# Kernel optimization log

Measured on AMD Instinct MI355X. Metric: run time of the kernel, lower is better.

## Reference

```python
import jax, jax.numpy as jnp
import numpy as np

B, H, N, D = 4, 16, 1024, 64


def setup_inputs() -> dict:
    key = jax.random.key(0)
    k1, k2, k3, k4, k5 = jax.random.split(key, 5)
    q = jax.random.normal(k1, (B, H, N, D), dtype=jnp.float32)
    k = jax.random.normal(k2, (B, H, N, D), dtype=jnp.float32)
    v = jax.random.normal(k3, (B, H, N, D), dtype=jnp.float32)
    # 1x1 Conv2d(heads, heads) weights -> [out_heads, in_heads]
    fan = 1.0 / np.sqrt(H)
    W_pre = jax.random.uniform(k4, (H, H), dtype=jnp.float32, minval=-fan, maxval=fan)
    W_post = jax.random.uniform(k5, (H, H), dtype=jnp.float32, minval=-fan, maxval=fan)
    return {"q": q, "k": k, "v": v, "W_pre": W_pre, "W_post": W_post}


def reference(q, k, v, W_pre, W_post):
    # q,k,v: [b, h, n, d]; talking-heads 1x1 conv mixes the head dim.
    scale = q.shape[-1] ** -0.5
    dots = jnp.einsum('bhid,bhjd->bhij', q, k) * scale
    # pre-softmax talking heads: out[g] = sum_h W_pre[g,h] * dots[h]
    dots = jnp.einsum('gh,bhij->bgij', W_pre, dots)
    n = dots.shape[-1]
    mask_value = -jnp.finfo(dots.dtype).max
    causal_mask = jnp.triu(jnp.ones((n, n), dtype=bool), k=1)  # [i, j]
    dots = jnp.where(causal_mask, mask_value, dots)
    # softmax computed in fp32 (qk_norm=False path), cast back to input dtype
    attn = jax.nn.softmax(dots.astype(jnp.float32), axis=-1).astype(dots.dtype)
    # post-softmax talking heads
    attn = jnp.einsum('gh,bhij->bgij', W_post, attn)
    out = jnp.einsum('bhij,bhjd->bhid', attn, v)
    return out
```

## Files before the change

### kernel.cpp

```cpp
#include <hip/hip_runtime.h>
#include <stdint.h>

#define B_  4
#define H_  16
#define N_  1024
#define D_  64
#define SS_R 328
#define A2_R 328

typedef _Float16 half4v __attribute__((ext_vector_type(4)));
typedef _Float16 half8v __attribute__((ext_vector_type(8)));
typedef float    f32x4  __attribute__((ext_vector_type(4)));

#define VT_OFF   0
#define VT_SZ    (B_ * H_ * D_ * N_ * 2)
#define LB_OFF   (VT_OFF + VT_SZ)
#define LB_SZ    (B_ * H_ * N_ * 4)
#define E_OFF    (LB_OFF + LB_SZ)
#define E_SZ     ((size_t)B_ * 2080 * 4096 * 2)
#define WS_NEED  ((size_t)E_OFF + E_SZ)

__device__ __forceinline__ half4v cvt4(f32x4 v) {
    half4v h;
    h[0] = (_Float16)v[0]; h[1] = (_Float16)v[1];
    h[2] = (_Float16)v[2]; h[3] = (_Float16)v[3];
    return h;
}

__device__ __forceinline__ int xcd_slot(int x) { return (x >> 3) + (x & 7) * 64; }

__global__ __launch_bounds__(256)
void prep_vt(const float* __restrict__ v, _Float16* __restrict__ VT) {
    __shared__ float T[64 * 67];
    const int t = threadIdx.x;
    const int bh = blockIdx.x >> 4, jb = blockIdx.x & 15, j0 = jb * 64;
    const float* src = v + ((size_t)bh * N_ + j0) * D_;
    #pragma unroll
    for (int m = 0; m < 4; ++m) {
        const int flat = m * 1024 + t * 4;
        const int j = flat >> 6, d0 = flat & 63;
        f32x4 val = *(const f32x4*)(src + flat);
        #pragma unroll
        for (int e = 0; e < 4; ++e) T[j * 67 + d0 + e] = val[e];
    }
    __syncthreads();
    const int d = t >> 2, jq = t & 3;
    half8v a, b2;
    #pragma unroll
    for (int jj = 0; jj < 8; ++jj) a[jj]  = (_Float16)T[(16 * jq + jj) * 67 + d];
    #pragma unroll
    for (int jj = 0; jj < 8; ++jj) b2[jj] = (_Float16)T[(16 * jq + 8 + jj) * 67 + d];
    _Float16* dst = VT + ((size_t)bh * D_ + d) * N_ + j0 + jq * 16;
    *(half8v*)dst = a;
    *(half8v*)(dst + 8) = b2;
}

__global__ __launch_bounds__(512, 2)
void attend_sweep1(const float* __restrict__ q, const float* __restrict__ k,
                   const float* __restrict__ Wpre, float* __restrict__ lbuf,
                   _Float16* __restrict__ Ebuf) {
    __shared__ _Float16 Ss[2][32 * SS_R];

    const int slot = xcd_slot(blockIdx.x);
    const int b = slot >> 7;
    const int r7 = slot & 127;
    const int m = r7 >> 2, phase = r7 & 3;
    const int itA = m, itB = 63 - m;
    const int i0A = m * 16, i0B = itB * 16;
    const int triA = itA * (itA + 1) / 2, triB = itB * (itB + 1) / 2;

    const int t = threadIdx.x;
    const int lane = t & 63, w = t >> 6;
    const int l16 = lane & 15, lg = lane >> 4;
    const int h0 = 2 * w;
    const size_t bh0 = (size_t)b * H_;
    _Float16* Eb = Ebuf + (size_t)b * 2080 * 4096;

    const half4v wpre_f = cvt4(*(const f32x4*)(Wpre + l16 * 16 + 4 * lg));

    half4v qf[2][2][4];
    #pragma unroll
    for (int s = 0; s < 2; ++s) {
        const int i0s = s ? i0B : i0A;
        #pragma unroll
        for (int e = 0; e < 2; ++e) {
            const float* qrow = q + ((bh0 + h0 + e) * N_ + i0s + l16) * D_;
            #pragma unroll
            for (int kk = 0; kk < 4; ++kk) {
                f32x4 qv = *(const f32x4*)(qrow + kk * 16 + 4 * lg);
                half4v hv;
                #pragma unroll
                for (int xx = 0; xx < 4; ++xx) hv[xx] = (_Float16)(qv[xx] * 0.125f);
                qf[s][e][kk] = hv;
            }
        }
    }

    float lp[4][4];
    #pragma unroll
    for (int ss = 0; ss < 4; ++ss)
        #pragma unroll
        for (int r = 0; r < 4; ++r) lp[ss][r] = 0.f;

    const float* kbase0 = k + ((bh0 + h0 + 0) * N_ + l16) * D_ + 4 * lg;
    const float* kbase1 = k + ((bh0 + h0 + 1) * N_ + l16) * D_ + 4 * lg;

    #define JT_OF(m_) (2 * (phase + 4 * ((m_) >> 1)) + ((m_) & 1))

    int jt = JT_OF(0);
    if (jt <= itB) {
        int pbuf = 0;
        half4v kfc[2][4];
        #pragma unroll
        for (int kk = 0; kk < 4; ++kk) {
            kfc[0][kk] = cvt4(*(const f32x4*)(kbase0 + (size_t)jt * 16 * D_ + kk * 16));
            kfc[1][kk] = cvt4(*(const f32x4*)(kbase1 + (size_t)jt * 16 * D_ + kk * 16));
        }
        for (int m_ = 0; ; ++m_) {
            const bool actA = (jt <= itA);
            #pragma unroll
            for (int s = 0; s < 2; ++s) {
                if (s == 0 && !actA) continue;
                #pragma unroll
                for (int e = 0; e < 2; ++e) {
                    f32x4 acc = {0.f, 0.f, 0.f, 0.f};
                    #pragma unroll
                    for (int kk = 0; kk < 4; ++kk)
                        acc = __builtin_amdgcn_mfma_f32_16x16x16f16(qf[s][e][kk], kfc[e][kk], acc, 0, 0, 0);
                    #pragma unroll
                    for (int r = 0; r < 4; ++r)
                        Ss[pbuf][(s * 16 + 4 * lg + r) * SS_R + l16 * 20 + h0 + e] = (_Float16)acc[r];
                }
            }
            const int jn = JT_OF(m_ + 1);
            const bool have_next = (jn <= itB);
            half4v kfn[2][4];
            if (have_next) {
                #pragma unroll
                for (int kk = 0; kk < 4; ++kk) {
                    kfn[0][kk] = cvt4(*(const f32x4*)(kbase0 + (size_t)jn * 16 * D_ + kk * 16));
                    kfn[1][kk] = cvt4(*(const f32x4*)(kbase1 + (size_t)jn * 16 * D_ + kk * 16));
                }
            }
            __syncthreads();
            #pragma unroll
            for (int ss = 0; ss < 4; ++ss) {
                const int strip = ss >> 1;
                if (strip == 0 && !actA) continue;
                const int sii = (ss & 1) * 8 + w;
                const int its = strip ? itB : itA;
                const int tri = strip ? triB : triA;
                half4v sfrag = *(const half4v*)&Ss[pbuf][(strip * 16 + sii) * SS_R + l16 * 20 + 4 * lg];
                f32x4 z = {0.f, 0.f, 0.f, 0.f};
                f32x4 m1 = __builtin_amdgcn_mfma_f32_16x16x16f16(wpre_f, sfrag, z, 0, 0, 0);
                const bool ok = (jt < its) || (l16 <= sii);
                half4v ev;
                #pragma unroll
                for (int r = 0; r < 4; ++r) {
                    const float e_ = ok ? __expf(m1[r]) : 0.f;
                    lp[ss][r] += e_;
                    ev[r] = (_Float16)e_;
                }
                *(half4v*)(Eb + (size_t)(tri + jt) * 4096 + w * 512 + l16 * 32 + lg * 8 + (ss & 1) * 4) = ev;
            }
            pbuf ^= 1;
            if (!have_next) break;
            jt = jn;
            #pragma unroll
            for (int kk = 0; kk < 4; ++kk) {
                kfc[0][kk] = kfn[0][kk];
                kfc[1][kk] = kfn[1][kk];
            }
        }
    }
    #undef JT_OF

    #pragma unroll
    for (int ss = 0; ss < 4; ++ss) {
        const int strip = ss >> 1;
        const int sii = (ss & 1) * 8 + w;
        const int i0s = strip ? i0B : i0A;
        #pragma unroll
        for (int r = 0; r < 4; ++r) {
            float val = lp[ss][r];
            val += __shfl_xor(val, 1, 64);
            val += __shfl_xor(val, 2, 64);
            val += __shfl_xor(val, 4, 64);
            val += __shfl_xor(val, 8, 64);
            if (l16 == 0)
                atomicAdd(&lbuf[(bh0 + 4 * lg + r) * N_ + i0s + sii], val);
        }
    }
}

__global__ __launch_bounds__(512, 8)
void attend_sweep2(const _Float16* __restrict__ Ebuf, const _Float16* __restrict__ VT,
                   const float* __restrict__ Wpost, const float* __restrict__ lbuf,
                   float* __restrict__ out) {
    __shared__ _Float16 A2s[2][16 * A2_R];

    const int x = blockIdx.x;
    const int r_ = x >> 4;
    const int it = (r_ < 32) ? (63 - r_) : (r_ - 32);
    const int sub = x & 15;
    const int b = sub >> 2, dq = sub & 3;
    const int i0 = it * 16;

    const int t = threadIdx.x;
    const int lane = t & 63, w = t >> 6;
    const int l16 = lane & 15, lg = lane >> 4;
    const int h0 = 2 * w;
    const size_t bh0 = (size_t)b * H_;

    const half4v wpost_f = cvt4(*(const f32x4*)(Wpost + l16 * 16 + 4 * lg));

    float lrecip[2][4];
    #pragma unroll
    for (int ss = 0; ss < 2; ++ss) {
        const int sii = ss * 8 + w;
        #pragma unroll
        for (int r = 0; r < 4; ++r)
            lrecip[ss][r] = 1.0f / lbuf[(bh0 + 4 * lg + r) * N_ + i0 + sii];
    }

    const _Float16* Eb = Ebuf + ((size_t)b * 2080 + (size_t)it * (it + 1) / 2) * 4096
                       + w * 512 + l16 * 32 + lg * 8;
    const _Float16* vb0 = VT + ((bh0 + h0 + 0) * D_ + dq * 16 + l16) * (size_t)N_ + 4 * lg;
    const _Float16* vb1 = VT + ((bh0 + h0 + 1) * D_ + dq * 16 + l16) * (size_t)N_ + 4 * lg;

    f32x4 oacc[2];
    #pragma unroll
    for (int e = 0; e < 2; ++e) oacc[e] = (f32x4){0.f, 0.f, 0.f, 0.f};

    int pb = 0;
    half8v e0 = *(const half8v*)(Eb);
    half8v e1 = (it >= 1) ? *(const half8v*)(Eb + 4096) : e0;
    half4v vc[2];
    vc[0] = *(const half4v*)(vb0);
    vc[1] = *(const half4v*)(vb1);

    for (int jt = 0; jt <= it; ++jt) {
        half8v e2 = e1;
        if (jt + 2 <= it) e2 = *(const half8v*)(Eb + (size_t)(jt + 2) * 4096);
        half4v vn[2];
        if (jt + 1 <= it) {
            vn[0] = *(const half4v*)(vb0 + (jt + 1) * 16);
            vn[1] = *(const half4v*)(vb1 + (jt + 1) * 16);
        } else {
            vn[0] = vc[0]; vn[1] = vc[1];
        }
        #pragma unroll
        for (int ss = 0; ss < 2; ++ss) {
            const int sii = ss * 8 + w;
            half4v pf;
            #pragma unroll
            for (int r = 0; r < 4; ++r)
                pf[r] = (_Float16)((float)e0[ss * 4 + r] * lrecip[ss][r]);
            f32x4 z = {0.f, 0.f, 0.f, 0.f};
            f32x4 m2 = __builtin_amdgcn_mfma_f32_16x16x16f16(wpost_f, pf, z, 0, 0, 0);
            #pragma unroll
            for (int r = 0; r < 4; ++r)
                A2s[pb][(4 * lg + r) * A2_R + sii * 20 + l16] = (_Float16)m2[r];
        }
        __syncthreads();
        #pragma unroll
        for (int e = 0; e < 2; ++e) {
            const int g = h0 + e;
            half4v bfrag = *(const half4v*)&A2s[pb][g * A2_R + l16 * 20 + 4 * lg];
            oacc[e] = __builtin_amdgcn_mfma_f32_16x16x16f16(vc[e], bfrag, oacc[e], 0, 0, 0);
        }
        e0 = e1; e1 = e2;
        vc[0] = vn[0]; vc[1] = vn[1];
        pb ^= 1;
    }

    #pragma unroll
    for (int e = 0; e < 2; ++e) {
        float* orow = out + ((bh0 + h0 + e) * N_ + i0 + l16) * D_;
        *(f32x4*)&orow[dq * 16 + 4 * lg] = oacc[e];
    }
}

__global__ __launch_bounds__(512, 2)
void attend_fused(const float* __restrict__ q, const float* __restrict__ k,
                  const float* __restrict__ v, const float* __restrict__ Wpre,
                  const float* __restrict__ Wpost, float* __restrict__ out) {
    __shared__ _Float16 Ss[32 * SS_R];
    __shared__ _Float16 A2s[16 * 648];

    const int t = threadIdx.x;
    const int b = blockIdx.x >> 5;
    const int m = blockIdx.x & 31;
    const int itA = m, itB = 63 - m;
    const int i0A = m * 16, i0B = (63 - m) * 16;

    const int lane = t & 63, w = t >> 6;
    const int l16 = lane & 15, lg = lane >> 4;
    const int h0 = 2 * w;
    const size_t bh0 = (size_t)b * H_;

    const half4v wpre_f  = cvt4(*(const f32x4*)(Wpre  + l16 * 16 + 4 * lg));
    const half4v wpost_f = cvt4(*(const f32x4*)(Wpost + l16 * 16 + 4 * lg));

    half4v qf[2][2][4];
    #pragma unroll
    for (int s = 0; s < 2; ++s) {
        const int i0s = s ? i0B : i0A;
        #pragma unroll
        for (int e = 0; e < 2; ++e) {
            const float* qrow = q + ((bh0 + h0 + e) * N_ + i0s + l16) * D_;
            #pragma unroll
            for (int kk = 0; kk < 4; ++kk) {
                f32x4 qv = *(const f32x4*)(qrow + kk * 16 + 4 * lg);
                half4v hv;
                #pragma unroll
                for (int xx = 0; xx < 4; ++xx) hv[xx] = (_Float16)(qv[xx] * 0.125f);
                qf[s][e][kk] = hv;
            }
        }
    }

    float lp[4][4];
    #pragma unroll
    for (int ss = 0; ss < 4; ++ss)
        #pragma unroll
        for (int r = 0; r < 4; ++r) lp[ss][r] = 0.f;

    for (int jt = 0; jt <= itB; ++jt) {
        const int j0 = jt * 16;
        const bool actA = (jt <= itA);
        half4v kf[2][4];
        #pragma unroll
        for (int e = 0; e < 2; ++e) {
            const float* krow = k + ((bh0 + h0 + e) * N_ + j0 + l16) * D_ + 4 * lg;
            #pragma unroll
            for (int kk = 0; kk < 4; ++kk) kf[e][kk] = cvt4(*(const f32x4*)(krow + kk * 16));
        }
        #pragma unroll
        for (int s = 0; s < 2; ++s) {
            if (s == 0 && !actA) continue;
            #pragma unroll
            for (int e = 0; e < 2; ++e) {
                f32x4 acc = {0.f, 0.f, 0.f, 0.f};
                #pragma unroll
                for (int kk = 0; kk < 4; ++kk)
                    acc = __builtin_amdgcn_mfma_f32_16x16x16f16(qf[s][e][kk], kf[e][kk], acc, 0, 0, 0);
                #pragma unroll
                for (int r = 0; r < 4; ++r)
                    Ss[(s * 16 + 4 * lg + r) * SS_R + l16 * 20 + h0 + e] = (_Float16)acc[r];
            }
        }
        __syncthreads();
        #pragma unroll
        for (int ss = 0; ss < 4; ++ss) {
            const int strip = ss >> 1;
            if (strip == 0 && !actA) continue;
            const int sii = (ss & 1) * 8 + w;
            const int its = strip ? itB : itA;
            half4v sfrag = *(const half4v*)&Ss[(strip * 16 + sii) * SS_R + l16 * 20 + 4 * lg];
            f32x4 z = {0.f, 0.f, 0.f, 0.f};
            f32x4 m1 = __builtin_amdgcn_mfma_f32_16x16x16f16(wpre_f, sfrag, z, 0, 0, 0);
            if ((jt < its) || (l16 <= sii)) {
                #pragma unroll
                for (int r = 0; r < 4; ++r) lp[ss][r] += __expf(m1[r]);
            }
        }
        __syncthreads();
    }

    float lrec[4][4];
    #pragma unroll
    for (int ss = 0; ss < 4; ++ss)
        #pragma unroll
        for (int r = 0; r < 4; ++r) {
            float val = lp[ss][r];
            val += __shfl_xor(val, 1, 64);
            val += __shfl_xor(val, 2, 64);
            val += __shfl_xor(val, 4, 64);
            val += __shfl_xor(val, 8, 64);
            lrec[ss][r] = 1.0f / val;
        }

    f32x4 oacc[2][2][4];
    #pragma unroll
    for (int s = 0; s < 2; ++s)
        #pragma unroll
        for (int e = 0; e < 2; ++e)
            #pragma unroll
            for (int ds = 0; ds < 4; ++ds)
                oacc[s][e][ds] = (f32x4){0.f, 0.f, 0.f, 0.f};

    for (int jt = 0; jt <= itB; ++jt) {
        const int j0 = jt * 16;
        const bool actA = (jt <= itA);
        half4v kf[2][4];
        #pragma unroll
        for (int e = 0; e < 2; ++e) {
            const float* krow = k + ((bh0 + h0 + e) * N_ + j0 + l16) * D_ + 4 * lg;
            #pragma unroll
            for (int kk = 0; kk < 4; ++kk) kf[e][kk] = cvt4(*(const f32x4*)(krow + kk * 16));
        }
        half4v vf[2][4];
        #pragma unroll
        for (int e = 0; e < 2; ++e)
            #pragma unroll
            for (int ds = 0; ds < 4; ++ds) {
                f32x4 vv;
                #pragma unroll
                for (int xx = 0; xx < 4; ++xx)
                    vv[xx] = v[((bh0 + h0 + e) * N_ + j0 + 4 * lg + xx) * D_ + ds * 16 + l16];
                vf[e][ds] = cvt4(vv);
            }
        #pragma unroll
        for (int s = 0; s < 2; ++s) {
            if (s == 0 && !actA) continue;
            #pragma unroll
            for (int e = 0; e < 2; ++e) {
                f32x4 acc = {0.f, 0.f, 0.f, 0.f};
                #pragma unroll
                for (int kk = 0; kk < 4; ++kk)
                    acc = __builtin_amdgcn_mfma_f32_16x16x16f16(qf[s][e][kk], kf[e][kk], acc, 0, 0, 0);
                #pragma unroll
                for (int r = 0; r < 4; ++r)
                    Ss[(s * 16 + 4 * lg + r) * SS_R + l16 * 20 + h0 + e] = (_Float16)acc[r];
            }
        }
        __syncthreads();
        #pragma unroll
        for (int ss = 0; ss < 4; ++ss) {
            const int strip = ss >> 1;
            if (strip == 0 && !actA) continue;
            const int sii = (ss & 1) * 8 + w;
            const int its = strip ? itB : itA;
            half4v sfrag = *(const half4v*)&Ss[(strip * 16 + sii) * SS_R + l16 * 20 + 4 * lg];
            f32x4 z = {0.f, 0.f, 0.f, 0.f};
            f32x4 m1 = __builtin_amdgcn_mfma_f32_16x16x16f16(wpre_f, sfrag, z, 0, 0, 0);
            const bool ok = (jt < its) || (l16 <= sii);
            half4v pfrag;
            #pragma unroll
            for (int r = 0; r < 4; ++r)
                pfrag[r] = (_Float16)(ok ? __expf(m1[r]) * lrec[ss][r] : 0.f);
            f32x4 m2 = __builtin_amdgcn_mfma_f32_16x16x16f16(wpost_f, pfrag, z, 0, 0, 0);
            #pragma unroll
            for (int r = 0; r < 4; ++r)
                A2s[(4 * lg + r) * 648 + (strip * 16 + sii) * 20 + l16] = (_Float16)m2[r];
        }
        __syncthreads();
        #pragma unroll
        for (int s = 0; s < 2; ++s) {
            if (s == 0 && !actA) continue;
            #pragma unroll
            for (int e = 0; e < 2; ++e) {
                half4v bfrag = *(const half4v*)&A2s[(h0 + e) * 648 + (s * 16 + l16) * 20 + 4 * lg];
                #pragma unroll
                for (int ds = 0; ds < 4; ++ds)
                    oacc[s][e][ds] = __builtin_amdgcn_mfma_f32_16x16x16f16(vf[e][ds], bfrag, oacc[s][e][ds], 0, 0, 0);
            }
        }
    }

    #pragma unroll
    for (int s = 0; s < 2; ++s) {
        const int i0s = s ? i0B : i0A;
        #pragma unroll
        for (int e = 0; e < 2; ++e) {
            float* orow = out + ((bh0 + h0 + e) * N_ + i0s + l16) * D_;
            #pragma unroll
            for (int ds = 0; ds < 4; ++ds)
                *(f32x4*)&orow[ds * 16 + 4 * lg] = oacc[s][e][ds];
        }
    }
}

extern "C" void kernel_launch(void* const* d_in, const int* in_sizes, int n_in,
                              void* d_out, int out_size, void* d_ws, size_t ws_size,
                              hipStream_t stream) {
    const float* q     = (const float*)d_in[0];
    const float* k     = (const float*)d_in[1];
    const float* v     = (const float*)d_in[2];
    const float* Wpre  = (const float*)d_in[3];
    const float* Wpost = (const float*)d_in[4];
    float* out = (float*)d_out;
    _Float16* VT   = (_Float16*)((char*)d_ws + VT_OFF);
    float*    lbuf = (float*)((char*)d_ws + LB_OFF);
    _Float16* Ebuf = (_Float16*)((char*)d_ws + E_OFF);

    if (ws_size >= WS_NEED) {
        prep_vt<<<dim3(B_ * H_ * (N_ / 64)), dim3(256), 0, stream>>>(v, VT);
        hipMemsetAsync((char*)d_ws + LB_OFF, 0, LB_SZ, stream);
        attend_sweep1<<<dim3(512), dim3(512), 0, stream>>>(q, k, Wpre, lbuf, Ebuf);
        attend_sweep2<<<dim3(1024), dim3(512), 0, stream>>>(Ebuf, VT, Wpost, lbuf, out);
    } else {
        attend_fused<<<dim3(B_ * 32), dim3(512), 0, stream>>>(q, k, v, Wpre, Wpost, out);
    }
}
```

Measured before the change: 164.0 us.

## Pair causal row tiles in sweep2 to share V loads and balance work

Each sweep2 block now handles two query row tiles, m and 63-m, so every block does the same amount of causal work. The two tiles reuse the same V fragment loads and share one barrier per iteration, and the grid is halved to 512 blocks. The change removes the load imbalance between short and long rows and cuts redundant V traffic. In exchange it doubles LDS usage and register pressure, lowers the occupancy hint to 4, and drops the two-deep E prefetch and the V prefetch in favour of single-step lookahead.

```diff
diff --git a/kernel.cpp b/kernel.cpp
--- a/kernel.cpp
+++ b/kernel.cpp
@@ -193,18 +193,20 @@
     }
 }
 
-__global__ __launch_bounds__(512, 8)
+__global__ __launch_bounds__(512, 4)
 void attend_sweep2(const _Float16* __restrict__ Ebuf, const _Float16* __restrict__ VT,
                    const float* __restrict__ Wpost, const float* __restrict__ lbuf,
                    float* __restrict__ out) {
-    __shared__ _Float16 A2s[2][16 * A2_R];
+    __shared__ _Float16 A2sA[2][16 * A2_R];
+    __shared__ _Float16 A2sB[2][16 * A2_R];
 
     const int x = blockIdx.x;
-    const int r_ = x >> 4;
-    const int it = (r_ < 32) ? (63 - r_) : (r_ - 32);
+    const int xm = x >> 4;
+    const int m = (x < 256) ? xm : (31 - (xm & 15));
     const int sub = x & 15;
     const int b = sub >> 2, dq = sub & 3;
-    const int i0 = it * 16;
+    const int itA = m, itB = 63 - m;
+    const int i0A = m * 16, i0B = itB * 16;
 
     const int t = threadIdx.x;
     const int lane = t & 63, w = t >> 6;
@@ -214,70 +216,95 @@
 
     const half4v wpost_f = cvt4(*(const f32x4*)(Wpost + l16 * 16 + 4 * lg));
 
-    float lrecip[2][4];
+    float lrA[2][4], lrB[2][4];
     #pragma unroll
     for (int ss = 0; ss < 2; ++ss) {
         const int sii = ss * 8 + w;
         #pragma unroll
-        for (int r = 0; r < 4; ++r)
-            lrecip[ss][r] = 1.0f / lbuf[(bh0 + 4 * lg + r) * N_ + i0 + sii];
-    }
-
-    const _Float16* Eb = Ebuf + ((size_t)b * 2080 + (size_t)it * (it + 1) / 2) * 4096
-                       + w * 512 + l16 * 32 + lg * 8;
+        for (int r = 0; r < 4; ++r) {
+            lrA[ss][r] = 1.0f / lbuf[(bh0 + 4 * lg + r) * N_ + i0A + sii];
+            lrB[ss][r] = 1.0f / lbuf[(bh0 + 4 * lg + r) * N_ + i0B + sii];
+        }
+    }
+
+    const size_t lane_off = (size_t)w * 512 + l16 * 32 + lg * 8;
+    const _Float16* EbA = Ebuf + ((size_t)b * 2080 + (size_t)itA * (itA + 1) / 2) * 4096 + lane_off;
+    const _Float16* EbB = Ebuf + ((size_t)b * 2080 + (size_t)itB * (itB + 1) / 2) * 4096 + lane_off;
     const _Float16* vb0 = VT + ((bh0 + h0 + 0) * D_ + dq * 16 + l16) * (size_t)N_ + 4 * lg;
     const _Float16* vb1 = VT + ((bh0 + h0 + 1) * D_ + dq * 16 + l16) * (size_t)N_ + 4 * lg;
 
-    f32x4 oacc[2];
-    #pragma unroll
-    for (int e = 0; e < 2; ++e) oacc[e] = (f32x4){0.f, 0.f, 0.f, 0.f};
+    f32x4 oaccA[2], oaccB[2];
+    #pragma unroll
+    for (int e = 0; e < 2; ++e) {
+        oaccA[e] = (f32x4){0.f, 0.f, 0.f, 0.f};
+        oaccB[e] = (f32x4){0.f, 0.f, 0.f, 0.f};
+    }
 
     int pb = 0;
-    half8v e0 = *(const half8v*)(Eb);
-    half8v e1 = (it >= 1) ? *(const half8v*)(Eb + 4096) : e0;
-    half4v vc[2];
-    vc[0] = *(const half4v*)(vb0);
-    vc[1] = *(const half4v*)(vb1);
-
-    for (int jt = 0; jt <= it; ++jt) {
-        half8v e2 = e1;
-        if (jt + 2 <= it) e2 = *(const half8v*)(Eb + (size_t)(jt + 2) * 4096);
-        half4v vn[2];
-        if (jt + 1 <= it) {
-            vn[0] = *(const half4v*)(vb0 + (jt + 1) * 16);
-            vn[1] = *(const half4v*)(vb1 + (jt + 1) * 16);
-        } else {
-            vn[0] = vc[0]; vn[1] = vc[1];
-        }
+    half8v eB = *(const half8v*)(EbB);
+    half8v eA = *(const half8v*)(EbA);
+
+    for (int jt = 0; jt <= itB; ++jt) {
+        const bool actA = (jt <= itA);
+        half4v vf[2];
+        vf[0] = *(const half4v*)(vb0 + jt * 16);
+        vf[1] = *(const half4v*)(vb1 + jt * 16);
+        half8v eBn = eB, eAn = eA;
+        if (jt < itB) eBn = *(const half8v*)(EbB + (size_t)(jt + 1) * 4096);
+        if (jt < itA) eAn = *(const half8v*)(EbA + (size_t)(jt + 1) * 4096);
         #pragma unroll
         for (int ss = 0; ss < 2; ++ss) {
             const int sii = ss * 8 + w;
             half4v pf;
             #pragma unroll
             for (int r = 0; r < 4; ++r)
-                pf[r] = (_Float16)((float)e0[ss * 4 + r] * lrecip[ss][r]);
+                pf[r] = (_Float16)((float)eB[ss * 4 + r] * lrB[ss][r]);
             f32x4 z = {0.f, 0.f, 0.f, 0.f};
             f32x4 m2 = __builtin_amdgcn_mfma_f32_16x16x16f16(wpost_f, pf, z, 0, 0, 0);
             #pragma unroll
             for (int r = 0; r < 4; ++r)
-                A2s[pb][(4 * lg + r) * A2_R + sii * 20 + l16] = (_Float16)m2[r];
+                A2sB[pb][(4 * lg + r) * A2_R + sii * 20 + l16] = (_Float16)m2[r];
+        }
+        if (actA) {
+            #pragma unroll
+            for (int ss = 0; ss < 2; ++ss) {
+                const int sii = ss * 8 + w;
+                half4v pf;
+                #pragma unroll
+                for (int r = 0; r < 4; ++r)
+                    pf[r] = (_Float16)((float)eA[ss * 4 + r] * lrA[ss][r]);
+                f32x4 z = {0.f, 0.f, 0.f, 0.f};
+                f32x4 m2 = __builtin_amdgcn_mfma_f32_16x16x16f16(wpost_f, pf, z, 0, 0, 0);
+                #pragma unroll
+                for (int r = 0; r < 4; ++r)
+                    A2sA[pb][(4 * lg + r) * A2_R + sii * 20 + l16] = (_Float16)m2[r];
+            }
         }
         __syncthreads();
         #pragma unroll
         for (int e = 0; e < 2; ++e) {
             const int g = h0 + e;
-            half4v bfrag = *(const half4v*)&A2s[pb][g * A2_R + l16 * 20 + 4 * lg];
-            oacc[e] = __builtin_amdgcn_mfma_f32_16x16x16f16(vc[e], bfrag, oacc[e], 0, 0, 0);
-        }
-        e0 = e1; e1 = e2;
-        vc[0] = vn[0]; vc[1] = vn[1];
+            half4v bfB = *(const half4v*)&A2sB[pb][g * A2_R + l16 * 20 + 4 * lg];
+            oaccB[e] = __builtin_amdgcn_mfma_f32_16x16x16f16(vf[e], bfB, oaccB[e], 0, 0, 0);
+        }
+        if (actA) {
+            #pragma unroll
+            for (int e = 0; e < 2; ++e) {
+                const int g = h0 + e;
+                half4v bfA = *(const half4v*)&A2sA[pb][g * A2_R + l16 * 20 + 4 * lg];
+                oaccA[e] = __builtin_amdgcn_mfma_f32_16x16x16f16(vf[e], bfA, oaccA[e], 0, 0, 0);
+            }
+        }
+        eB = eBn; eA = eAn;
         pb ^= 1;
     }
 
     #pragma unroll
     for (int e = 0; e < 2; ++e) {
-        float* orow = out + ((bh0 + h0 + e) * N_ + i0 + l16) * D_;
-        *(f32x4*)&orow[dq * 16 + 4 * lg] = oacc[e];
+        float* orowB = out + ((bh0 + h0 + e) * N_ + i0B + l16) * D_;
+        *(f32x4*)&orowB[dq * 16 + 4 * lg] = oaccB[e];
+        float* orowA = out + ((bh0 + h0 + e) * N_ + i0A + l16) * D_;
+        *(f32x4*)&orowA[dq * 16 + 4 * lg] = oaccA[e];
     }
 }
 
@@ -489,7 +516,7 @@
         prep_vt<<<dim3(B_ * H_ * (N_ / 64)), dim3(256), 0, stream>>>(v, VT);
         hipMemsetAsync((char*)d_ws + LB_OFF, 0, LB_SZ, stream);
         attend_sweep1<<<dim3(512), dim3(512), 0, stream>>>(q, k, Wpre, lbuf, Ebuf);
-        attend_sweep2<<<dim3(1024), dim3(512), 0, stream>>>(Ebuf, VT, Wpost, lbuf, out);
+        attend_sweep2<<<dim3(512), dim3(512), 0, stream>>>(Ebuf, VT, Wpost, lbuf, out);
     } else {
         attend_fused<<<dim3(B_ * 32), dim3(512), 0, stream>>>(q, k, v, Wpre, Wpost, out);
     }
```

Result: faster. 146.9 us, median of 3 (-10.4%).
